# Optimization experiments

Measured on AMD Instinct MI355X. Metric: run time of the kernel, lower is better.

## Reference

```python
import jax, jax.numpy as jnp
import numpy as np

E = 1024   # n_embd
H = 16     # n_heads
D = 64     # head_dim
G = 4      # n_kv_groups
F = 4096   # ffn hidden_dim
V = 32000  # vocab
L = 4      # n_layers (all full_attention)
B = 1
T = 2048
ROT = 16   # partial_rotary_factor 0.25 * head_dim 64, rounded to even
EPS = 1e-6
THETA = 10000.0


def rope_tables(seq_len):
    # matches compute_rope_params: inv_freq over even indices of rotary_dim
    inv_freq = 1.0 / (THETA ** (jnp.arange(0, ROT, 2, dtype=jnp.float32) / ROT))
    ang = jnp.arange(seq_len, dtype=jnp.float32)[:, None] * inv_freq[None, :]
    ang = jnp.concatenate([ang, ang], axis=1)  # [T, ROT]
    return jnp.cos(ang), jnp.sin(ang)


def rmsnorm(x, w):
    # torch RMSNorm: x * rsqrt(mean(x^2)+eps) * (1 + weight)
    xf = x.astype(jnp.float32)
    n = xf * jax.lax.rsqrt(jnp.mean(xf * xf, axis=-1, keepdims=True) + EPS)
    return (n * (1.0 + w)).astype(x.dtype)


def apply_rope(x, cos, sin):
    # x: [B, h, T, D]; cos/sin: [1, 1, T, ROT]; partial rotary on first ROT dims
    x_rot, x_pass = x[..., :ROT], x[..., ROT:]
    x1, x2 = x_rot[..., :ROT // 2], x_rot[..., ROT // 2:]
    rotated = jnp.concatenate([-x2, x1], axis=-1)
    return jnp.concatenate([x_rot * cos + rotated * sin, x_pass], axis=-1)


def _forward(tokens, emb, Wq, Wk, Wv, Wo, qn, kn, n1, n2, f1, f2, f3, fn, head):
    cos, sin = rope_tables(T)
    cos = cos[None, None]  # [1,1,T,ROT]
    sin = sin[None, None]
    mask = jnp.triu(jnp.ones((T, T), dtype=bool), k=1)  # True = masked
    scale = D ** -0.5
    x = emb[tokens]  # [B,T,E]

    def block(x, p):
        wq, wk, wv, wo, qw, kw, w1, w2, g1, g2, g3 = p
        h = rmsnorm(x, w1)
        # fused Q + gate projection -> [B,T,H,2D], chunk on last dim
        qg = (h @ wq).reshape(B, T, H, 2 * D)
        q = qg[..., :D].transpose(0, 2, 1, 3)            # [B,H,T,D]
        gate = qg[..., D:].reshape(B, T, H * D)          # [B,T,H*D]
        k = (h @ wk).reshape(B, T, G, D).transpose(0, 2, 1, 3)  # [B,G,T,D]
        v = (h @ wv).reshape(B, T, G, D).transpose(0, 2, 1, 3)
        q = rmsnorm(q, qw)
        k = rmsnorm(k, kw)
        q = apply_rope(q, cos, sin)
        k = apply_rope(k, cos, sin)
        k = jnp.repeat(k, H // G, axis=1)  # GQA expand -> [B,H,T,D]
        v = jnp.repeat(v, H // G, axis=1)
        scores = jnp.einsum('bhqd,bhkd->bhqk', q, k)
        scores = jnp.where(mask, -jnp.inf, scores) * scale
        w = jax.nn.softmax(scores.astype(jnp.float32), axis=-1).astype(q.dtype)
        ctx = jnp.einsum('bhqk,bhkd->bhqd', w, v)
        ctx = ctx.transpose(0, 2, 1, 3).reshape(B, T, H * D)
        ctx = ctx * jax.nn.sigmoid(gate)
        x = x + ctx @ wo
        h2 = rmsnorm(x, w2)
        ff = (jax.nn.silu(h2 @ g1) * (h2 @ g2)) @ g3
        return x + ff, None

    params = (Wq, Wk, Wv, Wo, qn, kn, n1, n2, f1, f2, f3)
    x, _ = jax.lax.scan(block, x, params)
    return rmsnorm(x, fn) @ head  # logits [B,T,V]


def setup_inputs() -> dict:
    key = jax.random.key(0)
    ks = jax.random.split(key, 16)
    s = 0.02
    rn = lambda k, shape, sc=s: jax.random.normal(k, shape, jnp.float32) * sc
    return {
        'tokens': jax.random.randint(ks[0], (B, T), 0, V),
        'emb': rn(ks[1], (V, E)),
        'Wq': rn(ks[2], (L, E, 2 * H * D)),
        'Wk': rn(ks[3], (L, E, G * D)),
        'Wv': rn(ks[4], (L, E, G * D)),
        'Wo': rn(ks[5], (L, H * D, E)),
        'qn': rn(ks[6], (L, D)),
        'kn': rn(ks[7], (L, D)),
        'n1': rn(ks[8], (L, E)),
        'n2': rn(ks[9], (L, E)),
        'f1': rn(ks[10], (L, E, F)),
        'f2': rn(ks[11], (L, E, F)),
        'f3': rn(ks[12], (L, F, E)),
        'fn': rn(ks[13], (E,)),
        'head': rn(ks[14], (E, V)),
    }


def reference(tokens, emb, Wq, Wk, Wv, Wo, qn, kn, n1, n2, f1, f2, f3, fn, head):
    return _forward(tokens, emb, Wq, Wk, Wv, Wo, qn, kn, n1, n2, f1, f2, f3, fn, head)
```

## Files before the change

### kernel.cpp

```cpp
#include <hip/hip_runtime.h>

#define T_LEN 2048
#define E_DIM 1024
#define H_N 16
#define G_N 4
#define D_H 64
#define F_DIM 4096
#define V_SZ 32000
#define L_N 4

typedef __attribute__((ext_vector_type(8))) __bf16 bf16x8;
typedef __attribute__((ext_vector_type(4))) float f32x4;

__device__ __forceinline__ unsigned short f2bf(float f){
  unsigned int u = __float_as_uint(f);
  unsigned int r = (u + 0x7FFFu + ((u >> 16) & 1u)) >> 16;
  return (unsigned short)r;
}

__device__ __forceinline__ f32x4 mfma16(bf16x8 a, bf16x8 b, f32x4 c){
  return __builtin_amdgcn_mfma_f32_16x16x32_bf16(a, b, c, 0, 0, 0);
}

__device__ __forceinline__ void gl16(const void* g, void* l){
  __builtin_amdgcn_global_load_lds((const __attribute__((address_space(1))) void*)g,
                                   (__attribute__((address_space(3))) void*)l, 16, 0, 0);
}

#define SBAR() __builtin_amdgcn_s_barrier()
#define LGK0() do{ asm volatile("s_waitcnt lgkmcnt(0)" ::: "memory"); __builtin_amdgcn_sched_barrier(0); }while(0)
#define VMC4() do{ asm volatile("s_waitcnt vmcnt(4)" ::: "memory"); __builtin_amdgcn_sched_barrier(0); }while(0)
#define VMC0() do{ asm volatile("s_waitcnt vmcnt(0)" ::: "memory"); __builtin_amdgcn_sched_barrier(0); }while(0)

__global__ __launch_bounds__(256) void embed_k(const float* __restrict__ emb,
                                               const int* __restrict__ tokens,
                                               float* __restrict__ x){
  int t = blockIdx.x;
  int tok = tokens[t];
  const float4* src = (const float4*)(emb + (size_t)tok * E_DIM);
  float4* dst = (float4*)(x + (size_t)t * E_DIM);
  dst[threadIdx.x] = src[threadIdx.x];
}

__global__ __launch_bounds__(256) void transpose_bf16(const float* __restrict__ src,
                                                      unsigned short* __restrict__ dst,
                                                      int R, int C){
  __shared__ float tile[32][33];
  int c0 = blockIdx.x * 32, r0 = blockIdx.y * 32;
  int tx = threadIdx.x & 31, ty = threadIdx.x >> 5;
  for (int i = 0; i < 4; i++){
    int r = ty + i * 8;
    tile[r][tx] = src[(size_t)(r0 + r) * C + c0 + tx];
  }
  __syncthreads();
  for (int i = 0; i < 4; i++){
    int r = ty + i * 8;
    dst[(size_t)(c0 + r) * R + r0 + tx] = f2bf(tile[tx][r]);
  }
}

__global__ __launch_bounds__(256) void rmsnorm_k(const float* __restrict__ x,
                                                 const float* __restrict__ w,
                                                 unsigned short* __restrict__ out){
  const int t = blockIdx.x, tid = threadIdx.x;
  const float4 v = ((const float4*)(x + (size_t)t * E_DIM))[tid];
  float ss = v.x*v.x + v.y*v.y + v.z*v.z + v.w*v.w;
  for (int m = 1; m < 64; m <<= 1) ss += __shfl_xor(ss, m);
  __shared__ float red[4];
  if ((tid & 63) == 0) red[tid >> 6] = ss;
  __syncthreads();
  ss = red[0] + red[1] + red[2] + red[3];
  const float r = rsqrtf(ss * (1.0f / E_DIM) + 1e-6f);
  const float4 wv = ((const float4*)w)[tid];
  ushort4 o;
  o.x = f2bf(v.x * r * (1.0f + wv.x));
  o.y = f2bf(v.y * r * (1.0f + wv.y));
  o.z = f2bf(v.z * r * (1.0f + wv.z));
  o.w = f2bf(v.w * r * (1.0f + wv.w));
  ((ushort4*)(out + (size_t)t * E_DIM))[tid] = o;
}

#define BM 128
#define BN 128
#define BK 32

template<bool ADD>
__global__ __launch_bounds__(256) void gemm_bt(const unsigned short* __restrict__ A,
                                               const unsigned short* __restrict__ Bt,
                                               float* __restrict__ C,
                                               int M, int N, int K){
  __shared__ unsigned short As[BM * BK];
  __shared__ unsigned short Bs[BN * BK];
  const int tid = threadIdx.x;
  const int lane = tid & 63, w = tid >> 6;
  const int wm = w >> 1, wn = w & 1;
  const int l15 = lane & 15, l4 = lane >> 4;

  const int chunk = gridDim.x >> 3;
  const int wgid = (blockIdx.x & 7) * chunk + (blockIdx.x >> 3);
  const int nm = M >> 7;
  const int bm = wgid % nm, bn = wgid / nm;
  const int m0 = bm * BM, n0 = bn * BN;

  const int r0 = tid >> 2;
  const int c0 = (tid & 3) << 3;

  const unsigned short* gA0 = A  + (size_t)(m0 + r0) * K + c0;
  const unsigned short* gA1 = A  + (size_t)(m0 + 64 + r0) * K + c0;
  const unsigned short* gB0 = Bt + (size_t)(n0 + r0) * K + c0;
  const unsigned short* gB1 = Bt + (size_t)(n0 + 64 + r0) * K + c0;
  unsigned short* lA0 = As + w * 512;
  unsigned short* lA1 = As + 2048 + w * 512;
  unsigned short* lB0 = Bs + w * 512;
  unsigned short* lB1 = Bs + 2048 + w * 512;

  f32x4 acc[4][4] = {};

  for (int k0 = 0; k0 < K; k0 += BK){
    __syncthreads();
    gl16(gA0 + k0, lA0);
    gl16(gA1 + k0, lA1);
    gl16(gB0 + k0, lB0);
    gl16(gB1 + k0, lB1);
    __syncthreads();
    bf16x8 af[4], bfr[4];
    for (int i = 0; i < 4; i++){
      af[i]  = *(const bf16x8*)&As[(wm * 64 + i * 16 + l15) * BK + l4 * 8];
      bfr[i] = *(const bf16x8*)&Bs[(wn * 64 + i * 16 + l15) * BK + l4 * 8];
    }
    for (int i = 0; i < 4; i++)
      for (int j = 0; j < 4; j++)
        acc[i][j] = mfma16(af[i], bfr[j], acc[i][j]);
  }

  for (int i = 0; i < 4; i++)
    for (int j = 0; j < 4; j++){
      int col = n0 + wn * 64 + j * 16 + l15;
      for (int r = 0; r < 4; r++){
        int row = m0 + wm * 64 + i * 16 + l4 * 4 + r;
        size_t idx = (size_t)row * N + col;
        if (ADD) C[idx] += acc[i][j][r]; else C[idx] = acc[i][j][r];
      }
    }
}

__global__ __launch_bounds__(512, 2) void gemm256(const unsigned short* __restrict__ A,
                                                  const unsigned short* __restrict__ Bt,
                                                  float* __restrict__ C,
                                                  int M, int N, int K){
  __shared__ unsigned short lds[65536];
  const int tid = threadIdx.x;
  const int lane = tid & 63, w = tid >> 6;
  const int wm = w >> 2, wn = w & 3;
  const int l15 = lane & 15, l4 = lane >> 4;

  const int chunk = gridDim.x >> 3;
  const int wgid = ((int)blockIdx.x & 7) * chunk + ((int)blockIdx.x >> 3);
  const int nm = M >> 8;
  const int bm = wgid % nm, bn = wgid / nm;
  const int m0 = bm * 256, n0 = bn * 256;
  const int NT = K >> 6;

  const int srow = (lane >> 3);
  const int scol = lane & 7;

  auto stageA = [&](int b, int h, int kt){
    #pragma unroll
    for (int c = 0; c < 2; c++){
      int r = w * 16 + c * 8 + srow;
      const unsigned short* g = A + (size_t)(m0 + h * 128 + r) * K + kt * 64 + ((scol ^ (r & 7)) << 3);
      gl16(g, (char*)lds + (b * 2 + h) * 16384 + (w * 16 + c * 8) * 128);
    }
  };
  auto stageB = [&](int b, int h, int kt){
    #pragma unroll
    for (int c = 0; c < 2; c++){
      int r = w * 16 + c * 8 + srow;
      const unsigned short* g = Bt + (size_t)(n0 + h * 128 + r) * K + kt * 64 + ((scol ^ (r & 7)) << 3);
      gl16(g, (char*)lds + 65536 + (b * 2 + h) * 16384 + (w * 16 + c * 8) * 128);
    }
  };

  const int sl0 = ((l4)     ^ (l15 & 7)) << 4;
  const int sl1 = ((4 | l4) ^ (l15 & 7)) << 4;

  f32x4 acc[8][4] = {};
  bf16x8 aF[8], bF[8];

  stageA(0, 0, 0); stageA(0, 1, 0); stageB(0, 0, 0); stageB(0, 1, 0);
  if (NT > 1){ stageB(1, 0, 1); stageB(1, 1, 1); }
  VMC4();
  SBAR();

  for (int kt = 0; kt < NT; kt++){
    const int buf = kt & 1;
    const char* Ab = (const char*)lds + (buf * 2 + wm) * 16384;
    const char* Bb = (const char*)lds + 65536 + (buf * 2 + (wn >> 1)) * 16384;
    const int brbase = (wn & 1) * 64;

    #pragma unroll
    for (int mf = 0; mf < 4; mf++){
      int r = mf * 16 + l15;
      aF[mf * 2 + 0] = *(const bf16x8*)(Ab + r * 128 + sl0);
      aF[mf * 2 + 1] = *(const bf16x8*)(Ab + r * 128 + sl1);
    }
    #pragma unroll
    for (int nf = 0; nf < 2; nf++){
      int r = brbase + nf * 16 + l15;
      bF[nf * 2 + 0] = *(const bf16x8*)(Bb + r * 128 + sl0);
      bF[nf * 2 + 1] = *(const bf16x8*)(Bb + r * 128 + sl1);
    }
    if (kt + 1 < NT) stageA(buf ^ 1, 0, kt + 1);
    SBAR(); LGK0();
    __builtin_amdgcn_s_setprio(1);
    #pragma unroll
    for (int mf = 0; mf < 4; mf++)
      #pragma unroll
      for (int nf = 0; nf < 2; nf++){
        acc[mf][nf] = mfma16(aF[mf * 2 + 0], bF[nf * 2 + 0], acc[mf][nf]);
        acc[mf][nf] = mfma16(aF[mf * 2 + 1], bF[nf * 2 + 1], acc[mf][nf]);
      }
    __builtin_amdgcn_s_setprio(0);
    SBAR();

    #pragma unroll
    for (int nf = 2; nf < 4; nf++){
      int r = brbase + nf * 16 + l15;
      bF[nf * 2 + 0] = *(const bf16x8*)(Bb + r * 128 + sl0);
      bF[nf * 2 + 1] = *(const bf16x8*)(Bb + r * 128 + sl1);
    }
    if (kt + 1 < NT) stageA(buf ^ 1, 1, kt + 1);
    SBAR(); LGK0();
    __builtin_amdgcn_s_setprio(1);
    #pragma unroll
    for (int mf = 0; mf < 4; mf++)
      #pragma unroll
      for (int nf = 2; nf < 4; nf++){
        acc[mf][nf] = mfma16(aF[mf * 2 + 0], bF[nf * 2 + 0], acc[mf][nf]);
        acc[mf][nf] = mfma16(aF[mf * 2 + 1], bF[nf * 2 + 1], acc[mf][nf]);
      }
    __builtin_amdgcn_s_setprio(0);
    SBAR();

    #pragma unroll
    for (int mf = 0; mf < 4; mf++){
      int r = 64 + mf * 16 + l15;
      aF[mf * 2 + 0] = *(const bf16x8*)(Ab + r * 128 + sl0);
      aF[mf * 2 + 1] = *(const bf16x8*)(Ab + r * 128 + sl1);
    }
    if (kt + 2 < NT) stageB(buf, 0, kt + 2);
    SBAR(); LGK0();
    __builtin_amdgcn_s_setprio(1);
    #pragma unroll
    for (int mf = 0; mf < 4; mf++)
      #pragma unroll
      for (int nf = 2; nf < 4; nf++){
        acc[4 + mf][nf] = mfma16(aF[mf * 2 + 0], bF[nf * 2 + 0], acc[4 + mf][nf]);
        acc[4 + mf][nf] = mfma16(aF[mf * 2 + 1], bF[nf * 2 + 1], acc[4 + mf][nf]);
      }
    __builtin_amdgcn_s_setprio(0);
    SBAR();

    if (kt + 2 < NT) stageB(buf, 1, kt + 2);
    SBAR();
    __builtin_amdgcn_s_setprio(1);
    #pragma unroll
    for (int mf = 0; mf < 4; mf++)
      #pragma unroll
      for (int nf = 0; nf < 2; nf++){
        acc[4 + mf][nf] = mfma16(aF[mf * 2 + 0], bF[nf * 2 + 0], acc[4 + mf][nf]);
        acc[4 + mf][nf] = mfma16(aF[mf * 2 + 1], bF[nf * 2 + 1], acc[4 + mf][nf]);
      }
    __builtin_amdgcn_s_setprio(0);
    if (kt + 2 < NT) { VMC4(); } else { VMC0(); }
    SBAR();
  }

  #pragma unroll
  for (int mfg = 0; mfg < 8; mfg++){
    #pragma unroll
    for (int nf = 0; nf < 4; nf++){
      int col = n0 + wn * 64 + nf * 16 + l15;
      int row0 = m0 + wm * 128 + mfg * 16 + l4 * 4;
      #pragma unroll
      for (int r = 0; r < 4; r++)
        C[(size_t)(row0 + r) * N + col] = acc[mfg][nf][r];
    }
  }
}

__global__ __launch_bounds__(256) void qkvpost_k(const float* __restrict__ qkv,
                                                 const float* __restrict__ qn,
                                                 const float* __restrict__ kn,
                                                 unsigned short* __restrict__ qb,
                                                 unsigned short* __restrict__ kb,
                                                 unsigned short* __restrict__ vt){
  const int t = blockIdx.x;
  const int lane = threadIdx.x & 63, w = threadIdx.x >> 6;
  const int d = lane;
  const int fi = d & 7;
  const float invf = powf(10000.0f, -(float)fi * 0.125f);
  const float ang = (float)t * invf;
  const float c = cosf(ang), s = sinf(ang);

  for (int i = 0; i < 4; i++){
    int h = w * 4 + i;
    float v = qkv[(size_t)t * 2560 + h * 128 + d];
    float ss = v * v;
    for (int m = 1; m < 64; m <<= 1) ss += __shfl_xor(ss, m);
    float r = rsqrtf(ss * (1.0f / D_H) + 1e-6f);
    float xn = v * r * (1.0f + qn[d]);
    float partner = __shfl_xor(xn, 8);
    float o;
    if (d < 8)       o = xn * c - partner * s;
    else if (d < 16) o = xn * c + partner * s;
    else             o = xn;
    qb[((size_t)h * T_LEN + t) * D_H + d] = f2bf(o);
  }
  {
    float v = qkv[(size_t)t * 2560 + 2048 + w * 64 + d];
    float ss = v * v;
    for (int m = 1; m < 64; m <<= 1) ss += __shfl_xor(ss, m);
    float r = rsqrtf(ss * (1.0f / D_H) + 1e-6f);
    float xn = v * r * (1.0f + kn[d]);
    float partner = __shfl_xor(xn, 8);
    float o;
    if (d < 8)       o = xn * c - partner * s;
    else if (d < 16) o = xn * c + partner * s;
    else             o = xn;
    kb[((size_t)w * T_LEN + t) * D_H + d] = f2bf(o);
  }
  {
    float v = qkv[(size_t)t * 2560 + 2304 + w * 64 + d];
    vt[((size_t)(w * 64 + d)) * T_LEN + t] = f2bf(v);
  }
}

__global__ __launch_bounds__(64) void attn_k(const unsigned short* __restrict__ qb,
                                             const unsigned short* __restrict__ kb,
                                             const unsigned short* __restrict__ vt,
                                             const float* __restrict__ qkv,
                                             unsigned short* __restrict__ ctxg){
  const int qt = blockIdx.x, h = blockIdx.y;
  const int g = h >> 2;
  const int lane = threadIdx.x;
  const int l15 = lane & 15, l4 = lane >> 4;
  const int q0 = qt * 16;
  __shared__ unsigned short Pl[16][40];

  const bf16x8 aq0 = *(const bf16x8*)(qb + ((size_t)h * T_LEN + q0 + l15) * D_H + l4 * 8);
  const bf16x8 aq1 = *(const bf16x8*)(qb + ((size_t)h * T_LEN + q0 + l15) * D_H + 32 + l4 * 8);

  f32x4 acc[4] = {};
  float mrun[4], lrun[4];
  for (int j = 0; j < 4; j++){ mrun[j] = -1e30f; lrun[j] = 0.0f; }

  for (int kv0 = 0; kv0 <= q0 + 15; kv0 += 32){
    f32x4 sc[2];
    for (int cp = 0; cp < 2; cp++){
      const unsigned short* kbase = kb + ((size_t)g * T_LEN + kv0 + cp * 16 + l15) * D_H + l4 * 8;
      bf16x8 bk0 = *(const bf16x8*)(kbase);
      bf16x8 bk1 = *(const bf16x8*)(kbase + 32);
      f32x4 z = {0.f, 0.f, 0.f, 0.f};
      z = mfma16(aq0, bk0, z);
      z = mfma16(aq1, bk1, z);
      sc[cp] = z;
    }
    float resc[4];
    for (int j = 0; j < 4; j++){
      int r = q0 + l4 * 4 + j;
      for (int cp = 0; cp < 2; cp++){
        int col = kv0 + cp * 16 + l15;
        float sv = sc[cp][j];
        sc[cp][j] = (col <= r) ? sv * 0.125f : -1e30f;
      }
      float mx = fmaxf(sc[0][j], sc[1][j]);
      for (int off = 1; off < 16; off <<= 1) mx = fmaxf(mx, __shfl_xor(mx, off));
      float mnew = fmaxf(mrun[j], mx);
      float p0 = __expf(sc[0][j] - mnew);
      float p1 = __expf(sc[1][j] - mnew);
      sc[0][j] = p0; sc[1][j] = p1;
      float sum = p0 + p1;
      for (int off = 1; off < 16; off <<= 1) sum += __shfl_xor(sum, off);
      resc[j] = __expf(mrun[j] - mnew);
      lrun[j] = lrun[j] * resc[j] + sum;
      mrun[j] = mnew;
    }
    __syncthreads();
    for (int j = 0; j < 4; j++){
      int r = l4 * 4 + j;
      Pl[r][l15]      = f2bf(sc[0][j]);
      Pl[r][16 + l15] = f2bf(sc[1][j]);
      for (int nt = 0; nt < 4; nt++) acc[nt][j] *= resc[j];
    }
    __syncthreads();
    bf16x8 pa = *(const bf16x8*)&Pl[l15][l4 * 8];
    for (int nt = 0; nt < 4; nt++){
      bf16x8 bv = *(const bf16x8*)(vt + ((size_t)g * 64 + nt * 16 + l15) * T_LEN + kv0 + l4 * 8);
      acc[nt] = mfma16(pa, bv, acc[nt]);
    }
  }

  for (int j = 0; j < 4; j++){
    int r = q0 + l4 * 4 + j;
    float inv = 1.0f / lrun[j];
    for (int nt = 0; nt < 4; nt++){
      int d = nt * 16 + l15;
      float gate = qkv[(size_t)r * 2560 + h * 128 + 64 + d];
      float val = acc[nt][j] * inv * (1.0f / (1.0f + __expf(-gate)));
      ctxg[(size_t)r * (H_N * D_H) + h * D_H + d] = f2bf(val);
    }
  }
}

__global__ __launch_bounds__(256) void silumul_k(const float* __restrict__ ff,
                                                 unsigned short* __restrict__ hg){
  size_t idx = ((size_t)blockIdx.x * 256 + threadIdx.x) * 4;
  size_t t = idx >> 12;
  size_t j = idx & 4095;
  const float4 u = *(const float4*)(ff + t * 8192 + j);
  const float4 gv = *(const float4*)(ff + t * 8192 + 4096 + j);
  ushort4 o;
  o.x = f2bf(u.x / (1.0f + __expf(-u.x)) * gv.x);
  o.y = f2bf(u.y / (1.0f + __expf(-u.y)) * gv.y);
  o.z = f2bf(u.z / (1.0f + __expf(-u.z)) * gv.z);
  o.w = f2bf(u.w / (1.0f + __expf(-u.w)) * gv.w);
  *(ushort4*)(hg + idx) = o;
}

extern "C" void kernel_launch(void* const* d_in, const int* in_sizes, int n_in,
                              void* d_out, int out_size, void* d_ws, size_t ws_size,
                              hipStream_t stream){
  (void)in_sizes; (void)n_in; (void)out_size; (void)ws_size;
  const int*   tokens = (const int*)d_in[0];
  const float* emb    = (const float*)d_in[1];
  const float* Wq     = (const float*)d_in[2];
  const float* Wk     = (const float*)d_in[3];
  const float* Wv     = (const float*)d_in[4];
  const float* Wo     = (const float*)d_in[5];
  const float* qn     = (const float*)d_in[6];
  const float* kn     = (const float*)d_in[7];
  const float* n1     = (const float*)d_in[8];
  const float* n2     = (const float*)d_in[9];
  const float* f1     = (const float*)d_in[10];
  const float* f2     = (const float*)d_in[11];
  const float* f3     = (const float*)d_in[12];
  const float* fn     = (const float*)d_in[13];
  const float* head   = (const float*)d_in[14];
  float* out = (float*)d_out;

  char* ws = (char*)d_ws;
  size_t off = 0;
  auto alloc = [&](size_t bytes)->char*{
    char* p = ws + off;
    off += (bytes + 255) & ~(size_t)255;
    return p;
  };
  float*          x       = (float*)alloc((size_t)T_LEN * E_DIM * 4);
  unsigned short* hbf     = (unsigned short*)alloc((size_t)T_LEN * E_DIM * 2);
  float*          qkvf    = (float*)alloc((size_t)T_LEN * 2560 * 4);
  unsigned short* qb      = (unsigned short*)alloc((size_t)H_N * T_LEN * D_H * 2);
  unsigned short* kb      = (unsigned short*)alloc((size_t)G_N * T_LEN * D_H * 2);
  unsigned short* vt      = (unsigned short*)alloc((size_t)G_N * D_H * T_LEN * 2);
  unsigned short* ctxg    = (unsigned short*)alloc((size_t)T_LEN * E_DIM * 2);
  float*          ff12    = (float*)alloc((size_t)T_LEN * 2 * F_DIM * 4);
  unsigned short* hg      = (unsigned short*)alloc((size_t)T_LEN * F_DIM * 2);
  unsigned short* wt_qkv  = (unsigned short*)alloc((size_t)2560 * E_DIM * 2);
  unsigned short* wt_o    = (unsigned short*)alloc((size_t)E_DIM * E_DIM * 2);
  unsigned short* wt_f12  = (unsigned short*)alloc((size_t)2 * F_DIM * E_DIM * 2);
  unsigned short* wt_f3   = (unsigned short*)alloc((size_t)E_DIM * F_DIM * 2);
  unsigned short* wt_head = (unsigned short*)alloc((size_t)V_SZ * E_DIM * 2);

  embed_k<<<T_LEN, 256, 0, stream>>>(emb, tokens, x);
  transpose_bf16<<<dim3(V_SZ / 32, E_DIM / 32), 256, 0, stream>>>(head, wt_head, E_DIM, V_SZ);

  for (int l = 0; l < L_N; l++){
    transpose_bf16<<<dim3(2048 / 32, 32), 256, 0, stream>>>(Wq + (size_t)l * E_DIM * 2048, wt_qkv, E_DIM, 2048);
    transpose_bf16<<<dim3(256 / 32, 32), 256, 0, stream>>>(Wk + (size_t)l * E_DIM * 256, wt_qkv + (size_t)2048 * E_DIM, E_DIM, 256);
    transpose_bf16<<<dim3(256 / 32, 32), 256, 0, stream>>>(Wv + (size_t)l * E_DIM * 256, wt_qkv + (size_t)2304 * E_DIM, E_DIM, 256);
    transpose_bf16<<<dim3(32, 32), 256, 0, stream>>>(Wo + (size_t)l * E_DIM * E_DIM, wt_o, E_DIM, E_DIM);
    transpose_bf16<<<dim3(F_DIM / 32, 32), 256, 0, stream>>>(f1 + (size_t)l * E_DIM * F_DIM, wt_f12, E_DIM, F_DIM);
    transpose_bf16<<<dim3(F_DIM / 32, 32), 256, 0, stream>>>(f2 + (size_t)l * E_DIM * F_DIM, wt_f12 + (size_t)F_DIM * E_DIM, E_DIM, F_DIM);
    transpose_bf16<<<dim3(E_DIM / 32, F_DIM / 32), 256, 0, stream>>>(f3 + (size_t)l * F_DIM * E_DIM, wt_f3, F_DIM, E_DIM);

    rmsnorm_k<<<T_LEN, 256, 0, stream>>>(x, n1 + l * E_DIM, hbf);
    gemm_bt<false><<<(T_LEN / BM) * (2560 / BN), 256, 0, stream>>>(hbf, wt_qkv, qkvf, T_LEN, 2560, E_DIM);
    qkvpost_k<<<T_LEN, 256, 0, stream>>>(qkvf, qn + l * D_H, kn + l * D_H, qb, kb, vt);
    attn_k<<<dim3(T_LEN / 16, H_N), 64, 0, stream>>>(qb, kb, vt, qkvf, ctxg);
    gemm_bt<true><<<(T_LEN / BM) * (E_DIM / BN), 256, 0, stream>>>(ctxg, wt_o, x, T_LEN, E_DIM, E_DIM);

    rmsnorm_k<<<T_LEN, 256, 0, stream>>>(x, n2 + l * E_DIM, hbf);
    gemm256<<<(T_LEN / 256) * (2 * F_DIM / 256), 512, 0, stream>>>(hbf, wt_f12, ff12, T_LEN, 2 * F_DIM, E_DIM);
    silumul_k<<<(T_LEN * F_DIM) / (256 * 4), 256, 0, stream>>>(ff12, hg);
    gemm_bt<true><<<(T_LEN / BM) * (E_DIM / BN), 256, 0, stream>>>(hg, wt_f3, x, T_LEN, E_DIM, F_DIM);
  }

  rmsnorm_k<<<T_LEN, 256, 0, stream>>>(x, fn, hbf);
  gemm256<<<(T_LEN / 256) * (V_SZ / 256), 512, 0, stream>>>(hbf, wt_head, out, T_LEN, V_SZ, E_DIM);
}
```

Before: 1.709 ms.

## Use 64x128 GEMM tiles and widen attention KV step with exp2 softmax

Replaces the 128x128 GEMM tile with a 64x128 tile, doubling the block count for the QKV, output-projection and FFN-down GEMMs so the GPU's compute units stay busier on these small problems. The attention kernel now processes 64 keys per iteration instead of 32. It folds the softmax scale and log2(e) into Q at preprocessing so it can use exp2f, and defers the row-sum shuffle reduction to the end. The trade-off is less data reuse per GEMM tile and more register pressure in attention, plus bf16 rounding of the pre-scaled Q.

Result: no change. 1.676 ms (-2.0%).

```diff
diff --git a/kernel.cpp b/kernel.cpp
--- a/kernel.cpp
+++ b/kernel.cpp
@@ -31,6 +31,8 @@
 #define LGK0() do{ asm volatile("s_waitcnt lgkmcnt(0)" ::: "memory"); __builtin_amdgcn_sched_barrier(0); }while(0)
 #define VMC4() do{ asm volatile("s_waitcnt vmcnt(4)" ::: "memory"); __builtin_amdgcn_sched_barrier(0); }while(0)
 #define VMC0() do{ asm volatile("s_waitcnt vmcnt(0)" ::: "memory"); __builtin_amdgcn_sched_barrier(0); }while(0)
+
+#define QSCALE 0.1803368801111183f
 
 __global__ __launch_bounds__(256) void embed_k(const float* __restrict__ emb,
                                                const int* __restrict__ tokens,
@@ -80,64 +82,56 @@
   ((ushort4*)(out + (size_t)t * E_DIM))[tid] = o;
 }
 
-#define BM 128
-#define BN 128
-#define BK 32
-
 template<bool ADD>
-__global__ __launch_bounds__(256) void gemm_bt(const unsigned short* __restrict__ A,
-                                               const unsigned short* __restrict__ Bt,
-                                               float* __restrict__ C,
-                                               int M, int N, int K){
-  __shared__ unsigned short As[BM * BK];
-  __shared__ unsigned short Bs[BN * BK];
+__global__ __launch_bounds__(256) void gemm64_bt(const unsigned short* __restrict__ A,
+                                                 const unsigned short* __restrict__ Bt,
+                                                 float* __restrict__ C,
+                                                 int M, int N, int K){
+  __shared__ unsigned short As[64 * 32];
+  __shared__ unsigned short Bs[128 * 32];
   const int tid = threadIdx.x;
   const int lane = tid & 63, w = tid >> 6;
-  const int wm = w >> 1, wn = w & 1;
   const int l15 = lane & 15, l4 = lane >> 4;
 
   const int chunk = gridDim.x >> 3;
   const int wgid = (blockIdx.x & 7) * chunk + (blockIdx.x >> 3);
-  const int nm = M >> 7;
+  const int nm = M >> 6;
   const int bm = wgid % nm, bn = wgid / nm;
-  const int m0 = bm * BM, n0 = bn * BN;
+  const int m0 = bm * 64, n0 = bn * 128;
 
   const int r0 = tid >> 2;
   const int c0 = (tid & 3) << 3;
 
-  const unsigned short* gA0 = A  + (size_t)(m0 + r0) * K + c0;
-  const unsigned short* gA1 = A  + (size_t)(m0 + 64 + r0) * K + c0;
+  const unsigned short* gA  = A  + (size_t)(m0 + r0) * K + c0;
   const unsigned short* gB0 = Bt + (size_t)(n0 + r0) * K + c0;
   const unsigned short* gB1 = Bt + (size_t)(n0 + 64 + r0) * K + c0;
-  unsigned short* lA0 = As + w * 512;
-  unsigned short* lA1 = As + 2048 + w * 512;
+  unsigned short* lA  = As + w * 512;
   unsigned short* lB0 = Bs + w * 512;
   unsigned short* lB1 = Bs + 2048 + w * 512;
 
-  f32x4 acc[4][4] = {};
-
-  for (int k0 = 0; k0 < K; k0 += BK){
+  f32x4 acc[4][2] = {};
+
+  for (int k0 = 0; k0 < K; k0 += 32){
     __syncthreads();
-    gl16(gA0 + k0, lA0);
-    gl16(gA1 + k0, lA1);
+    gl16(gA  + k0, lA);
     gl16(gB0 + k0, lB0);
     gl16(gB1 + k0, lB1);
     __syncthreads();
-    bf16x8 af[4], bfr[4];
-    for (int i = 0; i < 4; i++){
-      af[i]  = *(const bf16x8*)&As[(wm * 64 + i * 16 + l15) * BK + l4 * 8];
-      bfr[i] = *(const bf16x8*)&Bs[(wn * 64 + i * 16 + l15) * BK + l4 * 8];
-    }
+    bf16x8 af[4], bfr[2];
     for (int i = 0; i < 4; i++)
-      for (int j = 0; j < 4; j++)
+      af[i] = *(const bf16x8*)&As[(i * 16 + l15) * 32 + l4 * 8];
+    for (int j = 0; j < 2; j++)
+      bfr[j] = *(const bf16x8*)&Bs[(w * 32 + j * 16 + l15) * 32 + l4 * 8];
+    for (int i = 0; i < 4; i++)
+      for (int j = 0; j < 2; j++)
         acc[i][j] = mfma16(af[i], bfr[j], acc[i][j]);
   }
 
   for (int i = 0; i < 4; i++)
-    for (int j = 0; j < 4; j++){
-      int col = n0 + wn * 64 + j * 16 + l15;
+    for (int j = 0; j < 2; j++){
+      int col = n0 + w * 32 + j * 16 + l15;
       for (int r = 0; r < 4; r++){
-        int row = m0 + wm * 64 + i * 16 + l4 * 4 + r;
+        int row = m0 + i * 16 + l4 * 4 + r;
         size_t idx = (size_t)row * N + col;
         if (ADD) C[idx] += acc[i][j][r]; else C[idx] = acc[i][j][r];
       }
@@ -315,7 +309,7 @@
     if (d < 8)       o = xn * c - partner * s;
     else if (d < 16) o = xn * c + partner * s;
     else             o = xn;
-    qb[((size_t)h * T_LEN + t) * D_H + d] = f2bf(o);
+    qb[((size_t)h * T_LEN + t) * D_H + d] = f2bf(o * QSCALE);
   }
   {
     float v = qkv[(size_t)t * 2560 + 2048 + w * 64 + d];
@@ -346,18 +340,19 @@
   const int lane = threadIdx.x;
   const int l15 = lane & 15, l4 = lane >> 4;
   const int q0 = qt * 16;
-  __shared__ unsigned short Pl[16][40];
+  __shared__ unsigned short Pl[16][72];
 
   const bf16x8 aq0 = *(const bf16x8*)(qb + ((size_t)h * T_LEN + q0 + l15) * D_H + l4 * 8);
   const bf16x8 aq1 = *(const bf16x8*)(qb + ((size_t)h * T_LEN + q0 + l15) * D_H + 32 + l4 * 8);
 
   f32x4 acc[4] = {};
-  float mrun[4], lrun[4];
-  for (int j = 0; j < 4; j++){ mrun[j] = -1e30f; lrun[j] = 0.0f; }
-
-  for (int kv0 = 0; kv0 <= q0 + 15; kv0 += 32){
-    f32x4 sc[2];
-    for (int cp = 0; cp < 2; cp++){
+  float mrun[4], lpart[4];
+  for (int j = 0; j < 4; j++){ mrun[j] = -1e30f; lpart[j] = 0.0f; }
+
+  for (int kv0 = 0; kv0 <= q0 + 15; kv0 += 64){
+    f32x4 sc[4];
+    #pragma unroll
+    for (int cp = 0; cp < 4; cp++){
       const unsigned short* kbase = kb + ((size_t)g * T_LEN + kv0 + cp * 16 + l15) * D_H + l4 * 8;
       bf16x8 bk0 = *(const bf16x8*)(kbase);
       bf16x8 bk1 = *(const bf16x8*)(kbase + 32);
@@ -367,43 +362,57 @@
       sc[cp] = z;
     }
     float resc[4];
+    #pragma unroll
     for (int j = 0; j < 4; j++){
       int r = q0 + l4 * 4 + j;
-      for (int cp = 0; cp < 2; cp++){
+      #pragma unroll
+      for (int cp = 0; cp < 4; cp++){
         int col = kv0 + cp * 16 + l15;
-        float sv = sc[cp][j];
-        sc[cp][j] = (col <= r) ? sv * 0.125f : -1e30f;
-      }
-      float mx = fmaxf(sc[0][j], sc[1][j]);
+        sc[cp][j] = (col <= r) ? sc[cp][j] : -1e30f;
+      }
+      float mx = fmaxf(fmaxf(sc[0][j], sc[1][j]), fmaxf(sc[2][j], sc[3][j]));
       for (int off = 1; off < 16; off <<= 1) mx = fmaxf(mx, __shfl_xor(mx, off));
       float mnew = fmaxf(mrun[j], mx);
-      float p0 = __expf(sc[0][j] - mnew);
-      float p1 = __expf(sc[1][j] - mnew);
-      sc[0][j] = p0; sc[1][j] = p1;
-      float sum = p0 + p1;
-      for (int off = 1; off < 16; off <<= 1) sum += __shfl_xor(sum, off);
-      resc[j] = __expf(mrun[j] - mnew);
-      lrun[j] = lrun[j] * resc[j] + sum;
+      resc[j] = exp2f(mrun[j] - mnew);
       mrun[j] = mnew;
+      float ssum = 0.0f;
+      #pragma unroll
+      for (int cp = 0; cp < 4; cp++){
+        float pv = exp2f(sc[cp][j] - mnew);
+        sc[cp][j] = pv;
+        ssum += pv;
+      }
+      lpart[j] = lpart[j] * resc[j] + ssum;
+      #pragma unroll
+      for (int nt = 0; nt < 4; nt++) acc[nt][j] *= resc[j];
     }
     __syncthreads();
-    for (int j = 0; j < 4; j++){
-      int r = l4 * 4 + j;
-      Pl[r][l15]      = f2bf(sc[0][j]);
-      Pl[r][16 + l15] = f2bf(sc[1][j]);
-      for (int nt = 0; nt < 4; nt++) acc[nt][j] *= resc[j];
-    }
+    #pragma unroll
+    for (int j = 0; j < 4; j++)
+      #pragma unroll
+      for (int cp = 0; cp < 4; cp++)
+        Pl[l4 * 4 + j][cp * 16 + l15] = f2bf(sc[cp][j]);
     __syncthreads();
-    bf16x8 pa = *(const bf16x8*)&Pl[l15][l4 * 8];
+    const bf16x8 pa0 = *(const bf16x8*)&Pl[l15][l4 * 8];
+    const bf16x8 pa1 = *(const bf16x8*)&Pl[l15][32 + l4 * 8];
+    #pragma unroll
     for (int nt = 0; nt < 4; nt++){
-      bf16x8 bv = *(const bf16x8*)(vt + ((size_t)g * 64 + nt * 16 + l15) * T_LEN + kv0 + l4 * 8);
-      acc[nt] = mfma16(pa, bv, acc[nt]);
-    }
-  }
-
+      const unsigned short* vbase = vt + ((size_t)g * 64 + nt * 16 + l15) * T_LEN + kv0;
+      bf16x8 bv0 = *(const bf16x8*)(vbase + l4 * 8);
+      bf16x8 bv1 = *(const bf16x8*)(vbase + 32 + l4 * 8);
+      acc[nt] = mfma16(pa1, bv1, mfma16(pa0, bv0, acc[nt]));
+    }
+  }
+
+  #pragma unroll
+  for (int j = 0; j < 4; j++)
+    for (int off = 1; off < 16; off <<= 1) lpart[j] += __shfl_xor(lpart[j], off);
+
+  #pragma unroll
   for (int j = 0; j < 4; j++){
     int r = q0 + l4 * 4 + j;
-    float inv = 1.0f / lrun[j];
+    float inv = 1.0f / lpart[j];
+    #pragma unroll
     for (int nt = 0; nt < 4; nt++){
       int d = nt * 16 + l15;
       float gate = qkv[(size_t)r * 2560 + h * 128 + 64 + d];
@@ -484,15 +493,15 @@
     transpose_bf16<<<dim3(E_DIM / 32, F_DIM / 32), 256, 0, stream>>>(f3 + (size_t)l * F_DIM * E_DIM, wt_f3, F_DIM, E_DIM);
 
     rmsnorm_k<<<T_LEN, 256, 0, stream>>>(x, n1 + l * E_DIM, hbf);
-    gemm_bt<false><<<(T_LEN / BM) * (2560 / BN), 256, 0, stream>>>(hbf, wt_qkv, qkvf, T_LEN, 2560, E_DIM);
+    gemm64_bt<false><<<(T_LEN / 64) * (2560 / 128), 256, 0, stream>>>(hbf, wt_qkv, qkvf, T_LEN, 2560, E_DIM);
     qkvpost_k<<<T_LEN, 256, 0, stream>>>(qkvf, qn + l * D_H, kn + l * D_H, qb, kb, vt);
     attn_k<<<dim3(T_LEN / 16, H_N), 64, 0, stream>>>(qb, kb, vt, qkvf, ctxg);
-    gemm_bt<true><<<(T_LEN / BM) * (E_DIM / BN), 256, 0, stream>>>(ctxg, wt_o, x, T_LEN, E_DIM, E_DIM);
+    gemm64_bt<true><<<(T_LEN / 64) * (E_DIM / 128), 256, 0, stream>>>(ctxg, wt_o, x, T_LEN, E_DIM, E_DIM);
 
     rmsnorm_k<<<T_LEN, 256, 0, stream>>>(x, n2 + l * E_DIM, hbf);
     gemm256<<<(T_LEN / 256) * (2 * F_DIM / 256), 512, 0, stream>>>(hbf, wt_f12, ff12, T_LEN, 2 * F_DIM, E_DIM);
     silumul_k<<<(T_LEN * F_DIM) / (256 * 4), 256, 0, stream>>>(ff12, hg);
-    gemm_bt<true><<<(T_LEN / BM) * (E_DIM / BN), 256, 0, stream>>>(hg, wt_f3, x, T_LEN, E_DIM, F_DIM);
+    gemm64_bt<true><<<(T_LEN / 64) * (E_DIM / 128), 256, 0, stream>>>(hg, wt_f3, x, T_LEN, E_DIM, F_DIM);
   }
 
   rmsnorm_k<<<T_LEN, 256, 0, stream>>>(x, fn, hbf);
```
